# Optimization experiments

Measured on AMD Instinct MI355X. Metric: run time of the kernel, lower is better.

Reference implementation:

```python
import jax, jax.numpy as jnp
import numpy as np

EOS_ID = 1
E = 512
VS = 50000
VT = 50000
S_LEN = 128
T_LEN = 128


def setup_inputs() -> dict:
    key = jax.random.key(0)
    ks = jax.random.split(key, 16)
    sc = 0.05
    inp = {
        'source_words': jax.random.randint(ks[0], (S_LEN,), 0, VS, dtype=jnp.int64 if jax.config.jax_enable_x64 else jnp.int32),
        'target_words': jax.random.randint(ks[1], (T_LEN,), 0, VT, dtype=jnp.int64 if jax.config.jax_enable_x64 else jnp.int32),
        'W_x_hi': jax.random.normal(ks[2], (VS, E), jnp.float32) * sc,
        'W_y_hi': jax.random.normal(ks[3], (VT, E), jnp.float32) * sc,
        'enc_W_ih': jax.random.normal(ks[4], (4 * E, E), jnp.float32) * sc,
        'enc_W_hh': jax.random.normal(ks[5], (4 * E, E), jnp.float32) * sc,
        'enc_b_ih': jax.random.normal(ks[6], (4 * E,), jnp.float32) * sc,
        'enc_b_hh': jax.random.normal(ks[7], (4 * E,), jnp.float32) * sc,
        'dec_W_ih': jax.random.normal(ks[8], (4 * E, E), jnp.float32) * sc,
        'dec_W_hh': jax.random.normal(ks[9], (4 * E, E), jnp.float32) * sc,
        'dec_b_ih': jax.random.normal(ks[10], (4 * E,), jnp.float32) * sc,
        'dec_b_hh': jax.random.normal(ks[11], (4 * E,), jnp.float32) * sc,
        'W_hr_y': jax.random.normal(ks[12], (VT, E), jnp.float32) * sc,
        'b_hr_y': jax.random.normal(ks[13], (VT,), jnp.float32) * sc,
    }
    return inp


def _lstm_cell(x, h, c, W_ih, W_hh, b_ih, b_hh):
    # torch LSTMCell gate order: input, forget, cell(g), output
    gates = x @ W_ih.T + b_ih + h @ W_hh.T + b_hh  # [4E]
    i, f, g, o = jnp.split(gates, 4)
    c_new = jax.nn.sigmoid(f) * c + jax.nn.sigmoid(i) * jnp.tanh(g)
    h_new = jax.nn.sigmoid(o) * jnp.tanh(c_new)
    return h_new, c_new


def reference(source_words, target_words, W_x_hi, W_y_hi,
              enc_W_ih, enc_W_hh, enc_b_ih, enc_b_hh,
              dec_W_ih, dec_W_hh, dec_b_ih, dec_b_hh,
              W_hr_y, b_hr_y):
    e = W_x_hi.shape[1]
    h0 = jnp.zeros((e,), W_x_hi.dtype)

    # ---- encode: one LSTMCell step per source token ----
    def enc_step(carry, tok):
        h, c = carry
        x = W_x_hi[tok]
        return _lstm_cell(x, h, c, enc_W_ih, enc_W_hh, enc_b_ih, enc_b_hh), None

    (h, _c), _ = jax.lax.scan(enc_step, (h0, h0), source_words)

    # cell state is reset to zeros before decoding (as in the torch code)
    c = jnp.zeros_like(h)

    # ---- decode with teacher forcing; targets = target_words ++ [EOS] ----
    targets = jnp.concatenate([target_words, jnp.array([EOS_ID], target_words.dtype)])
    hi0 = W_x_hi[EOS_ID]  # first decoder input uses the SOURCE embedding of EOS

    def dec_step(carry, tok):
        h, c, hi = carry
        h, c = _lstm_cell(hi, h, c, dec_W_ih, dec_W_hh, dec_b_ih, dec_b_hh)
        logits = W_hr_y @ h + b_hr_y                       # [VT]
        loss = -jax.nn.log_softmax(logits)[tok]            # CE, batch=1 mean
        hi_next = W_y_hi[tok]
        return (h, c, hi_next), loss

    _, losses = jax.lax.scan(dec_step, (h, c, hi0), targets)
    return jnp.sum(losses)
```

## Files before the change

kernel.cpp:

```cpp
#include <hip/hip_runtime.h>
#include <cfloat>
#include <cmath>

#define E      512
#define FOURE  2048
#define VT     50000
#define SLEN   128
#define TLEN   129
#define NSTEPS 257
#define NB     64
#define NINBOX 32
#define NCHUNK 196
#define TPAD   132

#define INBOX_OFF  0
#define GXE_OFF    262144
#define PM_OFF     262144
#define PS_OFF     365632
#define TL_OFF     469120
#define HALL_OFF   786432
#define GXD_OFF    1310720

__device__ __forceinline__ float sigf(float x){ return 1.0f/(1.0f+__expf(-x)); }
__device__ __forceinline__ float tanhf_fast(float x){ return 2.f*sigf(2.f*x) - 1.f; }

__global__ __launch_bounds__(256) void gx_kernel(
    const int* __restrict__ src, const int* __restrict__ tgt,
    const float* __restrict__ Wx, const float* __restrict__ Wy,
    const float* __restrict__ encWih, const float* __restrict__ encBih, const float* __restrict__ encBhh,
    const float* __restrict__ decWih, const float* __restrict__ decBih, const float* __restrict__ decBhh,
    float* __restrict__ GxE, float* __restrict__ GxD)
{
  __shared__ float xs[8][E];
  const int tid  = threadIdx.x;
  const int tile = blockIdx.x;
  const bool is_dec = tile >= 16;
  const int t0 = is_dec ? (tile-16)*8 : tile*8;
  const int T  = is_dec ? TLEN : SLEN;

  for (int tt=0; tt<8; ++tt){
    int t = t0+tt;
    if (t < T){
      const float* xrow;
      if (is_dec) xrow = (t==0) ? (Wx + (size_t)1*E) : (Wy + (size_t)tgt[t-1]*E);
      else        xrow = Wx + (size_t)src[t]*E;
      xs[tt][tid]     = xrow[tid];
      xs[tt][tid+256] = xrow[tid+256];
    }
  }
  __syncthreads();

  const int r = blockIdx.y*256 + tid;
  const float* wrow = (is_dec ? decWih : encWih) + (size_t)r*E;
  const float  bias = is_dec ? (decBih[r]+decBhh[r]) : (encBih[r]+encBhh[r]);
  float acc[8];
  #pragma unroll
  for (int i=0;i<8;++i) acc[i]=0.f;

  for (int kc=0; kc<E; kc+=4){
    float4 w = *(const float4*)(wrow+kc);
    #pragma unroll
    for (int tt=0; tt<8; ++tt){
      float4 x = *(const float4*)&xs[tt][kc];
      acc[tt] += w.x*x.x + w.y*x.y + w.z*x.z + w.w*x.w;
    }
  }
  float* Gx = is_dec ? GxD : GxE;
  #pragma unroll
  for (int tt=0; tt<8; ++tt){
    int t = t0+tt;
    if (t < T) Gx[(size_t)t*FOURE + r] = bias + acc[tt];
  }
}

__device__ __forceinline__ void load_weights(
    const float* __restrict__ Whh, float* __restrict__ wldsw, int j, int lane)
{
  #pragma unroll
  for (int gg=0; gg<4; ++gg){
    const float* wr = Whh + (size_t)(gg*E + j)*E;
    float4 a = *(const float4*)(wr + 4*lane);
    float4 b = *(const float4*)(wr + 4*lane + 256);
    float* dst = wldsw + (size_t)gg*E + (lane&7)*64 + (lane>>3)*4;
    *(float4*)dst      = a;
    *(float4*)(dst+32) = b;
  }
}

__global__ __launch_bounds__(512, 1) void lstm_kernel(
    const float* __restrict__ GxE, const float* __restrict__ GxD,
    const float* __restrict__ encWhh, const float* __restrict__ decWhh,
    unsigned long long* __restrict__ inboxes, float* __restrict__ h_all)
{
  __shared__ float wlds[8][4][E];
  __shared__ float hmir[2][576];
  const int tid  = threadIdx.x;
  const int lane = tid & 63, wave = tid >> 6, bid = blockIdx.x;
  const int g = lane >> 4, k = lane & 15;
  const int j = bid*8 + wave;
  const int row = g*E + j;
  const int slot  = wave*64 + lane;
  const int pslot = slot + 4*(slot>>5);
  float* wldsw = &wlds[wave][0][0];
  const unsigned long long* myslot = inboxes + (size_t)(bid>>1)*1024 + slot;

  load_weights(encWhh, wldsw, j, lane);
  float cst = 0.f;

  for (int s=0; s<NSTEPS; ++s){
    if (s == SLEN){
      load_weights(decWhh, wldsw, j, lane);
      cst = 0.f;
    }
    const bool isdec = s >= SLEN;
    const int tloc = isdec ? (s - SLEN) : s;
    float gx = (isdec ? GxD : GxE)[(size_t)tloc*FOURE + row];

    float acc = 0.f;
    if (s > 0){
      const int buf = s & 1;
      unsigned long long hu;
      const unsigned long long* hp = myslot + (size_t)buf*512;
      for (int spin=0; spin<(1<<16); ++spin){
        hu = __hip_atomic_load(hp, __ATOMIC_RELAXED, __HIP_MEMORY_SCOPE_AGENT);
        if (__all((unsigned)(hu>>32) == (unsigned)s)) break;
        __builtin_amdgcn_s_sleep(1);
      }
      hmir[buf][pslot] = __uint_as_float((unsigned)hu);
      __syncthreads();
      const float* hb = &hmir[buf][36*k];
      #pragma unroll
      for (int i=0;i<8;++i){
        float4 h4 = *(const float4*)(hb + 4*i);
        float4 wv = *(const float4*)&wldsw[(size_t)g*E + i*64 + 4*k];
        acc += wv.x*h4.x + wv.y*h4.y + wv.z*h4.z + wv.w*h4.w;
      }
      acc += __shfl_xor(acc,1); acc += __shfl_xor(acc,2);
      acc += __shfl_xor(acc,4); acc += __shfl_xor(acc,8);
    }

    float gv = acc + gx;
    float x1 = __shfl_xor(gv,16);
    float x2 = __shfl_xor(gv,32);
    float x3 = __shfl_xor(x1,32);
    float gi = (g==0)?gv:(g==1)?x1:(g==2)?x2:x3;
    float gf = (g==0)?x1:(g==1)?gv:(g==2)?x3:x2;
    float gg = (g==0)?x2:(g==1)?x3:(g==2)?gv:x1;
    float go = (g==0)?x3:(g==1)?x2:(g==2)?x1:gv;
    cst = sigf(gf)*cst + sigf(gi)*tanhf_fast(gg);
    float hnew = sigf(go)*tanhf_fast(cst);

    unsigned long long pk = ((unsigned long long)(unsigned)(s+1) << 32)
                          |  (unsigned long long)__float_as_uint(hnew);
    if (lane < NINBOX)
      __hip_atomic_store(inboxes + (size_t)lane*1024 + (size_t)((s+1)&1)*512 + j,
                         pk, __ATOMIC_RELAXED, __HIP_MEMORY_SCOPE_AGENT);
    if (isdec && lane==0) h_all[(size_t)tloc*E + j] = hnew;
  }
}

__global__ __launch_bounds__(128) void c1_kernel(
    const float* __restrict__ h_all, const float* __restrict__ W, const float* __restrict__ bvec,
    const int* __restrict__ tgt, float* __restrict__ pm, float* __restrict__ ps, float* __restrict__ tl)
{
  __shared__ float hst[32][E];
  const int tid  = threadIdx.x;
  const int wv   = tid >> 6, lane = tid & 63;
  const int chunk = blockIdx.x;
  const int t0    = blockIdx.y * 32;
  const int nt    = (t0 + 32 <= TLEN) ? 32 : (TLEN - t0);

  for (int idx = tid; idx < nt*(E/4); idx += 128)
    ((float4*)&hst[0][0])[idx] = ((const float4*)(h_all + (size_t)t0*E))[idx];
  __syncthreads();

  const int c0 = chunk*256 + tid;
  const int c1 = c0 + 128;
  const bool v0 = c0 < VT, v1 = c1 < VT;
  const float* w0 = W + (size_t)(v0 ? c0 : 0)*E;
  const float* w1 = W + (size_t)(v1 ? c1 : 0)*E;

  float acc0[32], acc1[32];
  #pragma unroll
  for (int i=0;i<32;++i){ acc0[i]=0.f; acc1[i]=0.f; }

  for (int kc=0; kc<E; kc+=4){
    float4 wa = *(const float4*)(w0+kc);
    float4 wb = *(const float4*)(w1+kc);
    #pragma unroll
    for (int tt=0; tt<32; ++tt){
      float4 h4 = *(const float4*)&hst[tt][kc];
      acc0[tt] += wa.x*h4.x + wa.y*h4.y + wa.z*h4.z + wa.w*h4.w;
      acc1[tt] += wb.x*h4.x + wb.y*h4.y + wb.z*h4.z + wb.w*h4.w;
    }
  }
  const float b0 = v0 ? bvec[c0] : 0.f;
  const float b1 = v1 ? bvec[c1] : 0.f;

  __syncthreads();
  float* red = &hst[0][0];

  #pragma unroll
  for (int tt=0; tt<32; ++tt){
    const bool act = tt < nt;
    float x0 = v0 ? acc0[tt]+b0 : -FLT_MAX;
    float x1 = v1 ? acc1[tt]+b1 : -FLT_MAX;
    float mx = fmaxf(x0,x1);
    #pragma unroll
    for (int off=1; off<64; off<<=1) mx = fmaxf(mx, __shfl_xor(mx, off));
    if (lane==0) red[wv] = mx;
    __syncthreads();
    mx = fmaxf(red[0], red[1]);
    float e = (v0 ? __expf(x0-mx) : 0.f) + (v1 ? __expf(x1-mx) : 0.f);
    #pragma unroll
    for (int off=1; off<64; off<<=1) e += __shfl_xor(e, off);
    if (lane==0) red[2+wv] = e;
    __syncthreads();
    float ssum = red[2] + red[3];
    if (act){
      int t = t0 + tt;
      if (tid==0){ pm[(size_t)chunk*TPAD + t] = mx; ps[(size_t)chunk*TPAD + t] = ssum; }
      int tok = (t < SLEN) ? tgt[t] : 1;
      if (v0 && c0==tok) tl[t] = x0;
      if (v1 && c1==tok) tl[t] = x1;
    }
    __syncthreads();
  }
}

__global__ __launch_bounds__(256) void c2_kernel(
    const float* __restrict__ pm, const float* __restrict__ ps, const float* __restrict__ tl,
    float* __restrict__ out)
{
  const int tid = threadIdx.x;
  float loss = 0.f;
  if (tid < TLEN){
    float m = -FLT_MAX, ssum = 0.f;
    for (int ch=0; ch<NCHUNK; ++ch){
      float mc = pm[(size_t)ch*TPAD + tid];
      float sc = ps[(size_t)ch*TPAD + tid];
      float nm = fmaxf(m, mc);
      ssum = ssum*__expf(m-nm) + sc*__expf(mc-nm);
      m = nm;
    }
    loss = (m + __logf(ssum)) - tl[tid];
  }
  __shared__ float red[4];
  #pragma unroll
  for (int off=1; off<64; off<<=1) loss += __shfl_xor(loss, off);
  if ((tid & 63)==0) red[tid>>6] = loss;
  __syncthreads();
  if (tid==0) out[0] = red[0]+red[1]+red[2]+red[3];
}

extern "C" void kernel_launch(void* const* d_in, const int* in_sizes, int n_in,
                              void* d_out, int out_size, void* d_ws, size_t ws_size,
                              hipStream_t stream)
{
  const int*   src    = (const int*)  d_in[0];
  const int*   tgt    = (const int*)  d_in[1];
  const float* Wx     = (const float*)d_in[2];
  const float* Wy     = (const float*)d_in[3];
  const float* encWih = (const float*)d_in[4];
  const float* encWhh = (const float*)d_in[5];
  const float* encBih = (const float*)d_in[6];
  const float* encBhh = (const float*)d_in[7];
  const float* decWih = (const float*)d_in[8];
  const float* decWhh = (const float*)d_in[9];
  const float* decBih = (const float*)d_in[10];
  const float* decBhh = (const float*)d_in[11];
  const float* Whr    = (const float*)d_in[12];
  const float* bhr    = (const float*)d_in[13];

  char* ws = (char*)d_ws;
  unsigned long long* inboxes = (unsigned long long*)(ws + INBOX_OFF);
  float* GxE    = (float*)(ws + GXE_OFF);
  float* GxD    = (float*)(ws + GXD_OFF);
  float* hall   = (float*)(ws + HALL_OFF);
  float* pm     = (float*)(ws + PM_OFF);
  float* ps     = (float*)(ws + PS_OFF);
  float* tl     = (float*)(ws + TL_OFF);

  hipMemsetAsync(ws + INBOX_OFF, 0, NINBOX*1024*8, stream);

  dim3 ggrid(33, 8);
  gx_kernel<<<ggrid, 256, 0, stream>>>(src, tgt, Wx, Wy,
      encWih, encBih, encBhh, decWih, decBih, decBhh, GxE, GxD);

  lstm_kernel<<<NB, 512, 0, stream>>>(GxE, GxD, encWhh, decWhh, inboxes, hall);

  dim3 cgrid(NCHUNK, 5);
  c1_kernel<<<cgrid, 128, 0, stream>>>(hall, Whr, bhr, tgt, pm, ps, tl);

  c2_kernel<<<1, 256, 0, stream>>>(pm, ps, tl, (float*)d_out);
}
```

Before: 1.124 ms.

## Fuse LSTM recurrence and vocab projection into one persistent kernel with progress flags

Merges the recurrent LSTM kernel and the output-projection/softmax kernel into a single launch. 64 blocks run the recurrence and publish per-step progress counters, and 245 extra blocks each handle a 32-timestep tile of the vocab projection. Each of those blocks waits until its timesteps' hidden states are written, so the projection of earlier decoder steps overlaps the remaining recurrence. This adds spin-waiting blocks that hold CUs, and it relies on all 309 blocks being co-resident to avoid deadlock. It also changes block shape for the projection (4 chunks per 512-thread block).

```diff
diff --git a/kernel.cpp b/kernel.cpp
--- a/kernel.cpp
+++ b/kernel.cpp
@@ -8,7 +8,9 @@
 #define SLEN   128
 #define TLEN   129
 #define NSTEPS 257
-#define NB     64
+#define NBL    64
+#define NC1    245
+#define NGRID  309
 #define NINBOX 32
 #define NCHUNK 196
 #define TPAD   132
@@ -20,6 +22,7 @@
 #define TL_OFF     469120
 #define HALL_OFF   786432
 #define GXD_OFF    1310720
+#define PROG_OFF   2367488
 
 __device__ __forceinline__ float sigf(float x){ return 1.0f/(1.0f+__expf(-x)); }
 __device__ __forceinline__ float tanhf_fast(float x){ return 2.f*sigf(2.f*x) - 1.f; }
@@ -73,7 +76,7 @@
   }
 }
 
-__device__ __forceinline__ void load_weights(
+__device__ __forceinline__ void load_weights_s(
     const float* __restrict__ Whh, float* __restrict__ wldsw, int j, int lane)
 {
   #pragma unroll
@@ -87,144 +90,168 @@
   }
 }
 
-__global__ __launch_bounds__(512, 1) void lstm_kernel(
+__global__ __launch_bounds__(512, 1) void mega_kernel(
     const float* __restrict__ GxE, const float* __restrict__ GxD,
     const float* __restrict__ encWhh, const float* __restrict__ decWhh,
-    unsigned long long* __restrict__ inboxes, float* __restrict__ h_all)
-{
-  __shared__ float wlds[8][4][E];
-  __shared__ float hmir[2][576];
-  const int tid  = threadIdx.x;
-  const int lane = tid & 63, wave = tid >> 6, bid = blockIdx.x;
-  const int g = lane >> 4, k = lane & 15;
-  const int j = bid*8 + wave;
-  const int row = g*E + j;
-  const int slot  = wave*64 + lane;
-  const int pslot = slot + 4*(slot>>5);
-  float* wldsw = &wlds[wave][0][0];
-  const unsigned long long* myslot = inboxes + (size_t)(bid>>1)*1024 + slot;
-
-  load_weights(encWhh, wldsw, j, lane);
-  float cst = 0.f;
-
-  for (int s=0; s<NSTEPS; ++s){
-    if (s == SLEN){
-      load_weights(decWhh, wldsw, j, lane);
-      cst = 0.f;
-    }
-    const bool isdec = s >= SLEN;
-    const int tloc = isdec ? (s - SLEN) : s;
-    float gx = (isdec ? GxD : GxE)[(size_t)tloc*FOURE + row];
-
-    float acc = 0.f;
-    if (s > 0){
-      const int buf = s & 1;
-      unsigned long long hu;
-      const unsigned long long* hp = myslot + (size_t)buf*512;
-      for (int spin=0; spin<(1<<16); ++spin){
-        hu = __hip_atomic_load(hp, __ATOMIC_RELAXED, __HIP_MEMORY_SCOPE_AGENT);
-        if (__all((unsigned)(hu>>32) == (unsigned)s)) break;
-        __builtin_amdgcn_s_sleep(1);
-      }
-      hmir[buf][pslot] = __uint_as_float((unsigned)hu);
-      __syncthreads();
-      const float* hb = &hmir[buf][36*k];
+    unsigned long long* __restrict__ inboxes, unsigned* __restrict__ h_all,
+    unsigned* __restrict__ prog,
+    const float* __restrict__ W, const float* __restrict__ bvec,
+    const int* __restrict__ tgt,
+    float* __restrict__ pm, float* __restrict__ ps, float* __restrict__ tl)
+{
+  __shared__ float smemf[17552];
+  const int tid = threadIdx.x;
+
+  if (blockIdx.x < NBL){
+    const int lane = tid & 63, wave = tid >> 6, bid = blockIdx.x;
+    const int g = lane >> 4, k = lane & 15;
+    const int j = bid*8 + wave;
+    const int row = g*E + j;
+    const int slot  = wave*64 + lane;
+    const int pslot = slot + 4*(slot>>5);
+    float* wldsw = smemf + wave*2048;
+    float* hmir  = smemf + 16384;
+    const unsigned long long* myslot = inboxes + (size_t)(bid>>1)*1024 + slot;
+
+    load_weights_s(encWhh, wldsw, j, lane);
+    float cst = 0.f;
+
+    for (int s=0; s<NSTEPS; ++s){
+      if (s == SLEN){
+        load_weights_s(decWhh, wldsw, j, lane);
+        cst = 0.f;
+      }
+      const bool isdec = s >= SLEN;
+      const int tloc = isdec ? (s - SLEN) : s;
+      float gx = (isdec ? GxD : GxE)[(size_t)tloc*FOURE + row];
+
+      float acc = 0.f;
+      if (s > 0){
+        const int buf = s & 1;
+        unsigned long long hu;
+        const unsigned long long* hp = myslot + (size_t)buf*512;
+        for (int spin=0; spin<(1<<16); ++spin){
+          hu = __hip_atomic_load(hp, __ATOMIC_RELAXED, __HIP_MEMORY_SCOPE_AGENT);
+          if (__all((unsigned)(hu>>32) == (unsigned)s)) break;
+          __builtin_amdgcn_s_sleep(1);
+        }
+        hmir[buf*576 + pslot] = __uint_as_float((unsigned)hu);
+        __syncthreads();
+        if (tid==0) atomicAdd(&prog[s*4], 1u);
+        const float* hb = hmir + buf*576 + 36*k;
+        #pragma unroll
+        for (int i=0;i<8;++i){
+          float4 h4 = *(const float4*)(hb + 4*i);
+          float4 wv = *(const float4*)&wldsw[(size_t)g*E + i*64 + 4*k];
+          acc += wv.x*h4.x + wv.y*h4.y + wv.z*h4.z + wv.w*h4.w;
+        }
+        acc += __shfl_xor(acc,1); acc += __shfl_xor(acc,2);
+        acc += __shfl_xor(acc,4); acc += __shfl_xor(acc,8);
+      }
+
+      float gv = acc + gx;
+      float x1 = __shfl_xor(gv,16);
+      float x2 = __shfl_xor(gv,32);
+      float x3 = __shfl_xor(x1,32);
+      float gi = (g==0)?gv:(g==1)?x1:(g==2)?x2:x3;
+      float gf = (g==0)?x1:(g==1)?gv:(g==2)?x3:x2;
+      float gg = (g==0)?x2:(g==1)?x3:(g==2)?gv:x1;
+      float go = (g==0)?x3:(g==1)?x2:(g==2)?x1:gv;
+      cst = sigf(gf)*cst + sigf(gi)*tanhf_fast(gg);
+      float hnew = sigf(go)*tanhf_fast(cst);
+
+      unsigned long long pk = ((unsigned long long)(unsigned)(s+1) << 32)
+                            |  (unsigned long long)__float_as_uint(hnew);
+      if (lane < NINBOX)
+        __hip_atomic_store(inboxes + (size_t)lane*1024 + (size_t)((s+1)&1)*512 + j,
+                           pk, __ATOMIC_RELAXED, __HIP_MEMORY_SCOPE_AGENT);
+      if (isdec && lane==0)
+        __hip_atomic_store(h_all + (size_t)tloc*E + j, __float_as_uint(hnew),
+                           __ATOMIC_RELAXED, __HIP_MEMORY_SCOPE_AGENT);
+    }
+    __syncthreads();
+    if (tid==0) atomicAdd(&prog[257*4], 1u);
+
+  } else {
+    const int bc   = blockIdx.x - NBL;
+    const int ty   = bc / 49;
+    const int sub  = tid >> 7;
+    const int stid = tid & 127;
+    const int chunk = (bc % 49)*4 + sub;
+    const int wv   = stid >> 6, lane = tid & 63;
+    const int t0   = ty * 32;
+    const int nt   = (t0 + 32 <= TLEN) ? 32 : (TLEN - t0);
+    float* hst  = smemf;
+    float* redm = smemf + 16384;
+    float* reds = smemf + 16392;
+
+    const int gate_s = (ty < 4) ? (160 + 32*ty) : 257;
+    if (tid == 0){
+      for (int spin=0; spin<(1<<22); ++spin){
+        if (__hip_atomic_load(&prog[gate_s*4], __ATOMIC_RELAXED, __HIP_MEMORY_SCOPE_AGENT)
+            >= (unsigned)NBL) break;
+        __builtin_amdgcn_s_sleep(16);
+      }
+    }
+    __syncthreads();
+
+    {
+      unsigned long long* hst64 = (unsigned long long*)hst;
+      const unsigned long long* hsrc = (const unsigned long long*)(h_all + (size_t)t0*E);
+      for (int i=tid; i<nt*(E/2); i+=512)
+        hst64[i] = __hip_atomic_load(hsrc+i, __ATOMIC_RELAXED, __HIP_MEMORY_SCOPE_AGENT);
+    }
+    __syncthreads();
+
+    const int c0 = chunk*256 + stid;
+    const int c1 = c0 + 128;
+    const bool v0 = c0 < VT, v1 = c1 < VT;
+    const float* w0 = W + (size_t)(v0 ? c0 : 0)*E;
+    const float* w1 = W + (size_t)(v1 ? c1 : 0)*E;
+
+    float acc0[32], acc1[32];
+    #pragma unroll
+    for (int i=0;i<32;++i){ acc0[i]=0.f; acc1[i]=0.f; }
+
+    for (int kc=0; kc<E; kc+=4){
+      float4 wa = *(const float4*)(w0+kc);
+      float4 wb = *(const float4*)(w1+kc);
       #pragma unroll
-      for (int i=0;i<8;++i){
-        float4 h4 = *(const float4*)(hb + 4*i);
-        float4 wv = *(const float4*)&wldsw[(size_t)g*E + i*64 + 4*k];
-        acc += wv.x*h4.x + wv.y*h4.y + wv.z*h4.z + wv.w*h4.w;
-      }
-      acc += __shfl_xor(acc,1); acc += __shfl_xor(acc,2);
-      acc += __shfl_xor(acc,4); acc += __shfl_xor(acc,8);
-    }
-
-    float gv = acc + gx;
-    float x1 = __shfl_xor(gv,16);
-    float x2 = __shfl_xor(gv,32);
-    float x3 = __shfl_xor(x1,32);
-    float gi = (g==0)?gv:(g==1)?x1:(g==2)?x2:x3;
-    float gf = (g==0)?x1:(g==1)?gv:(g==2)?x3:x2;
-    float gg = (g==0)?x2:(g==1)?x3:(g==2)?gv:x1;
-    float go = (g==0)?x3:(g==1)?x2:(g==2)?x1:gv;
-    cst = sigf(gf)*cst + sigf(gi)*tanhf_fast(gg);
-    float hnew = sigf(go)*tanhf_fast(cst);
-
-    unsigned long long pk = ((unsigned long long)(unsigned)(s+1) << 32)
-                          |  (unsigned long long)__float_as_uint(hnew);
-    if (lane < NINBOX)
-      __hip_atomic_store(inboxes + (size_t)lane*1024 + (size_t)((s+1)&1)*512 + j,
-                         pk, __ATOMIC_RELAXED, __HIP_MEMORY_SCOPE_AGENT);
-    if (isdec && lane==0) h_all[(size_t)tloc*E + j] = hnew;
-  }
-}
-
-__global__ __launch_bounds__(128) void c1_kernel(
-    const float* __restrict__ h_all, const float* __restrict__ W, const float* __restrict__ bvec,
-    const int* __restrict__ tgt, float* __restrict__ pm, float* __restrict__ ps, float* __restrict__ tl)
-{
-  __shared__ float hst[32][E];
-  const int tid  = threadIdx.x;
-  const int wv   = tid >> 6, lane = tid & 63;
-  const int chunk = blockIdx.x;
-  const int t0    = blockIdx.y * 32;
-  const int nt    = (t0 + 32 <= TLEN) ? 32 : (TLEN - t0);
-
-  for (int idx = tid; idx < nt*(E/4); idx += 128)
-    ((float4*)&hst[0][0])[idx] = ((const float4*)(h_all + (size_t)t0*E))[idx];
-  __syncthreads();
-
-  const int c0 = chunk*256 + tid;
-  const int c1 = c0 + 128;
-  const bool v0 = c0 < VT, v1 = c1 < VT;
-  const float* w0 = W + (size_t)(v0 ? c0 : 0)*E;
-  const float* w1 = W + (size_t)(v1 ? c1 : 0)*E;
-
-  float acc0[32], acc1[32];
-  #pragma unroll
-  for (int i=0;i<32;++i){ acc0[i]=0.f; acc1[i]=0.f; }
-
-  for (int kc=0; kc<E; kc+=4){
-    float4 wa = *(const float4*)(w0+kc);
-    float4 wb = *(const float4*)(w1+kc);
+      for (int tt=0; tt<32; ++tt){
+        float4 h4 = *(const float4*)&hst[tt*E + kc];
+        acc0[tt] += wa.x*h4.x + wa.y*h4.y + wa.z*h4.z + wa.w*h4.w;
+        acc1[tt] += wb.x*h4.x + wb.y*h4.y + wb.z*h4.z + wb.w*h4.w;
+      }
+    }
+    const float b0 = v0 ? bvec[c0] : 0.f;
+    const float b1 = v1 ? bvec[c1] : 0.f;
+
     #pragma unroll
     for (int tt=0; tt<32; ++tt){
-      float4 h4 = *(const float4*)&hst[tt][kc];
-      acc0[tt] += wa.x*h4.x + wa.y*h4.y + wa.z*h4.z + wa.w*h4.w;
-      acc1[tt] += wb.x*h4.x + wb.y*h4.y + wb.z*h4.z + wb.w*h4.w;
-    }
-  }
-  const float b0 = v0 ? bvec[c0] : 0.f;
-  const float b1 = v1 ? bvec[c1] : 0.f;
-
-  __syncthreads();
-  float* red = &hst[0][0];
-
-  #pragma unroll
-  for (int tt=0; tt<32; ++tt){
-    const bool act = tt < nt;
-    float x0 = v0 ? acc0[tt]+b0 : -FLT_MAX;
-    float x1 = v1 ? acc1[tt]+b1 : -FLT_MAX;
-    float mx = fmaxf(x0,x1);
-    #pragma unroll
-    for (int off=1; off<64; off<<=1) mx = fmaxf(mx, __shfl_xor(mx, off));
-    if (lane==0) red[wv] = mx;
-    __syncthreads();
-    mx = fmaxf(red[0], red[1]);
-    float e = (v0 ? __expf(x0-mx) : 0.f) + (v1 ? __expf(x1-mx) : 0.f);
-    #pragma unroll
-    for (int off=1; off<64; off<<=1) e += __shfl_xor(e, off);
-    if (lane==0) red[2+wv] = e;
-    __syncthreads();
-    float ssum = red[2] + red[3];
-    if (act){
-      int t = t0 + tt;
-      if (tid==0){ pm[(size_t)chunk*TPAD + t] = mx; ps[(size_t)chunk*TPAD + t] = ssum; }
-      int tok = (t < SLEN) ? tgt[t] : 1;
-      if (v0 && c0==tok) tl[t] = x0;
-      if (v1 && c1==tok) tl[t] = x1;
-    }
-    __syncthreads();
+      const bool act = tt < nt;
+      float x0 = v0 ? acc0[tt]+b0 : -FLT_MAX;
+      float x1 = v1 ? acc1[tt]+b1 : -FLT_MAX;
+      float mx = fmaxf(x0,x1);
+      #pragma unroll
+      for (int off=1; off<64; off<<=1) mx = fmaxf(mx, __shfl_xor(mx, off));
+      if (lane==0) redm[sub*2+wv] = mx;
+      __syncthreads();
+      mx = fmaxf(redm[sub*2], redm[sub*2+1]);
+      float e = (v0 ? __expf(x0-mx) : 0.f) + (v1 ? __expf(x1-mx) : 0.f);
+      #pragma unroll
+      for (int off=1; off<64; off<<=1) e += __shfl_xor(e, off);
+      if (lane==0) reds[sub*2+wv] = e;
+      __syncthreads();
+      float ssum = reds[sub*2] + reds[sub*2+1];
+      if (act){
+        int t = t0 + tt;
+        if (stid==0){ pm[(size_t)chunk*TPAD + t] = mx; ps[(size_t)chunk*TPAD + t] = ssum; }
+        int tok = (t < SLEN) ? tgt[t] : 1;
+        if (v0 && c0==tok) tl[t] = x0;
+        if (v1 && c1==tok) tl[t] = x1;
+      }
+      __syncthreads();
+    }
   }
 }
 
@@ -274,23 +301,23 @@
 
   char* ws = (char*)d_ws;
   unsigned long long* inboxes = (unsigned long long*)(ws + INBOX_OFF);
-  float* GxE    = (float*)(ws + GXE_OFF);
-  float* GxD    = (float*)(ws + GXD_OFF);
-  float* hall   = (float*)(ws + HALL_OFF);
-  float* pm     = (float*)(ws + PM_OFF);
-  float* ps     = (float*)(ws + PS_OFF);
-  float* tl     = (float*)(ws + TL_OFF);
+  float* GxE     = (float*)(ws + GXE_OFF);
+  float* GxD     = (float*)(ws + GXD_OFF);
+  unsigned* hall = (unsigned*)(ws + HALL_OFF);
+  unsigned* prog = (unsigned*)(ws + PROG_OFF);
+  float* pm      = (float*)(ws + PM_OFF);
+  float* ps      = (float*)(ws + PS_OFF);
+  float* tl      = (float*)(ws + TL_OFF);
 
   hipMemsetAsync(ws + INBOX_OFF, 0, NINBOX*1024*8, stream);
+  hipMemsetAsync(ws + PROG_OFF, 0, 258*16, stream);
 
   dim3 ggrid(33, 8);
   gx_kernel<<<ggrid, 256, 0, stream>>>(src, tgt, Wx, Wy,
       encWih, encBih, encBhh, decWih, decBih, decBhh, GxE, GxD);
 
-  lstm_kernel<<<NB, 512, 0, stream>>>(GxE, GxD, encWhh, decWhh, inboxes, hall);
-
-  dim3 cgrid(NCHUNK, 5);
-  c1_kernel<<<cgrid, 128, 0, stream>>>(hall, Whr, bhr, tgt, pm, ps, tl);
+  mega_kernel<<<NGRID, 512, 0, stream>>>(GxE, GxD, encWhh, decWhh,
+      inboxes, hall, prog, Whr, bhr, tgt, pm, ps, tl);
 
   c2_kernel<<<1, 256, 0, stream>>>(pm, ps, tl, (float*)d_out);
 }
```

After: 1.102 ms. -2.0%, faster.
